# Performance work log

Hardware: AMD Instinct MI355X
Metric: run time of the kernel (lower is better)

Reference implementation:

```python
import jax, jax.numpy as jnp
import numpy as np

B, T, C, H = 4, 2048, 768, 12
D = C // H  # head dim = 64


def setup_inputs() -> dict:
    key = jax.random.key(0)
    ks = jax.random.split(key, 4)
    scale = 0.02
    return {
        "x": jax.random.normal(ks[0], (B, T, C), dtype=jnp.float32),
        "W_attn": jax.random.normal(ks[1], (C, 3 * C), dtype=jnp.float32) * scale,
        "b_attn": jnp.zeros((3 * C,), dtype=jnp.float32),
        "W_proj": jax.random.normal(ks[2], (C, C), dtype=jnp.float32) * scale,
        "b_proj": jnp.zeros((C,), dtype=jnp.float32),
    }


def reference(x, W_attn, b_attn, W_proj, b_proj):
    Bsz, Tlen, Cdim = x.shape
    qkv = x @ W_attn + b_attn                    # [B,T,3C]
    q, k, v = jnp.split(qkv, 3, axis=-1)          # each [B,T,C]
    # [B,T,C] -> [B,H,T,D]
    def heads(t):
        return t.reshape(Bsz, Tlen, H, D).transpose(0, 2, 1, 3)
    q, k, v = heads(q), heads(k), heads(v)
    att = jnp.einsum("bhqd,bhkd->bhqk", q, k) * (1.0 / np.sqrt(D))
    # causal mask: position q attends to k <= q
    mask = jnp.tril(jnp.ones((Tlen, Tlen), dtype=bool))
    att = jnp.where(mask[None, None], att, -jnp.inf)
    att = jax.nn.softmax(att, axis=-1)
    y = jnp.einsum("bhqk,bhkd->bhqd", att, v)     # [B,H,T,D]
    y = y.transpose(0, 2, 1, 3).reshape(Bsz, Tlen, Cdim)
    return y @ W_proj + b_proj
```

## Files before the change

### kernel.cpp

```cpp
#include <hip/hip_runtime.h>

#define B_SZ   4
#define T_LEN  2048
#define C_DIM  768
#define H_NUM  12
#define THREEC (3 * C_DIM)

typedef _Float16 f16;
typedef _Float16 half8 __attribute__((ext_vector_type(8)));
typedef _Float16 half4 __attribute__((ext_vector_type(4)));
typedef __fp16   pk2   __attribute__((ext_vector_type(2)));
typedef float    f32x4 __attribute__((ext_vector_type(4)));

#define GLD16(gaddr, laddr)                                                         \
  __builtin_amdgcn_global_load_lds(                                                 \
      (const __attribute__((address_space(1))) unsigned int*)(gaddr),               \
      (__attribute__((address_space(3))) unsigned int*)(laddr), 16, 0, 0)
#define MFMA16(a, b, c) __builtin_amdgcn_mfma_f32_16x16x32_f16(a, b, c, 0, 0, 0)

__global__ __launch_bounds__(256) void cast_f32_f16_kernel(
    const float* __restrict__ src, f16* __restrict__ dst, int n8) {
  int i = blockIdx.x * 256 + threadIdx.x;
  if (i >= n8) return;
  const float* s = src + (size_t)i * 8;
  half8 h;
#pragma unroll
  for (int u = 0; u < 8; ++u) h[u] = (f16)s[u];
  *(half8*)(dst + (size_t)i * 8) = h;
}

__global__ __launch_bounds__(256) void transpose_cast2_kernel(
    const float* __restrict__ Wa, const float* __restrict__ Wp,
    f16* __restrict__ WtA, f16* __restrict__ WtP) {
  __shared__ f16 tile[32][33];
  int bx = blockIdx.x;
  const float* W; f16* Wt; int N;
  if (bx < THREEC / 32) { W = Wa; Wt = WtA; N = THREEC; }
  else { W = Wp; Wt = WtP; N = C_DIM; bx -= THREEC / 32; }
  const int n0 = bx * 32, k0 = blockIdx.y * 32;
  const int tx = threadIdx.x & 31, ty = threadIdx.x >> 5;
#pragma unroll
  for (int i = 0; i < 4; ++i)
    tile[ty + i * 8][tx] = (f16)W[(size_t)(k0 + ty + i * 8) * N + n0 + tx];
  __syncthreads();
#pragma unroll
  for (int i = 0; i < 4; ++i)
    Wt[(size_t)(n0 + ty + i * 8) * C_DIM + k0 + tx] = tile[tx][ty + i * 8];
}

template <int BM, int BN, int OUT_F16>
__global__ __launch_bounds__(256) void gemm_f16_kernel(
    const f16* __restrict__ A, const f16* __restrict__ Bt,
    const float* __restrict__ bias, f16* __restrict__ OutH,
    float* __restrict__ OutF, int M, int N, int K) {
  __shared__ f16 As[BM * 64];
  __shared__ f16 Bs[BN * 64];
  const int tid = threadIdx.x;
  const int lane = tid & 63, wave = tid >> 6;
  const int lm = lane & 15, kq = lane >> 4, lm7 = lm & 7;
  constexpr int MT = BM / 32, NT = BN / 32;
  const int wm = (wave & 1) * (BM / 2), wn = (wave >> 1) * (BN / 2);
  const int row0 = blockIdx.y * BM, col0 = blockIdx.x * BN;

  f32x4 acc[MT][NT] = {};

  for (int k0 = 0; k0 < K; k0 += 64) {
    __syncthreads();
#pragma unroll
    for (int i = 0; i < BM / 32; ++i) {
      int c = tid + i * 256;
      int r = c >> 3, cc = (c & 7) ^ (r & 7);
      GLD16(&A[(size_t)(row0 + r) * K + k0 + cc * 8],
            &As[(i * 256 + wave * 64) * 8]);
    }
#pragma unroll
    for (int i = 0; i < BN / 32; ++i) {
      int c = tid + i * 256;
      int r = c >> 3, cc = (c & 7) ^ (r & 7);
      GLD16(&Bt[(size_t)(col0 + r) * K + k0 + cc * 8],
            &Bs[(i * 256 + wave * 64) * 8]);
    }
    __syncthreads();
#pragma unroll
    for (int ks = 0; ks < 2; ++ks) {
      const int pos = (ks * 4 + kq);
      half8 af[MT], bf[NT];
#pragma unroll
      for (int t = 0; t < MT; ++t)
        af[t] = *(const half8*)&As[(wm + t * 16 + lm) * 64 + (pos ^ lm7) * 8];
#pragma unroll
      for (int t = 0; t < NT; ++t)
        bf[t] = *(const half8*)&Bs[(wn + t * 16 + lm) * 64 + (pos ^ lm7) * 8];
#pragma unroll
      for (int mt = 0; mt < MT; ++mt)
#pragma unroll
        for (int nt = 0; nt < NT; ++nt)
          acc[mt][nt] = MFMA16(af[mt], bf[nt], acc[mt][nt]);
    }
  }

#pragma unroll
  for (int mt = 0; mt < MT; ++mt) {
    const int row = row0 + wm + mt * 16 + kq * 4;
#pragma unroll
    for (int nt = 0; nt < NT; ++nt) {
      const int col = col0 + wn + nt * 16 + lm;
      const float bv = bias[col];
#pragma unroll
      for (int r = 0; r < 4; ++r) {
        float v = acc[mt][nt][r] + bv;
        if (OUT_F16)
          OutH[(size_t)(row + r) * N + col] = (f16)v;
        else
          OutF[(size_t)(row + r) * N + col] = v;
      }
    }
  }
}

__global__ __launch_bounds__(256) void v_transpose_kernel(
    const f16* __restrict__ qkv, f16* __restrict__ vt) {
  __shared__ f16 tile[64 * 68];
  const int bh = blockIdx.x, b = bh / H_NUM, h = bh % H_NUM;
  const int t0 = blockIdx.y * 64;
  const int tid = threadIdx.x;
#pragma unroll
  for (int i = 0; i < 2; ++i) {
    int c = tid + i * 256;
    int tr = c >> 3, doff = (c & 7) * 8;
    int pcol = ((tr >> 5) << 5) | (((tr >> 2) & 3) << 3) |
               (((tr >> 4) & 1) << 2) | (tr & 3);
    half8 v = *(const half8*)&qkv[(size_t)(b * T_LEN + t0 + tr) * THREEC + 2 * C_DIM + h * 64 + doff];
#pragma unroll
    for (int u = 0; u < 8; ++u) tile[(doff + u) * 68 + pcol] = v[u];
  }
  __syncthreads();
#pragma unroll
  for (int i = 0; i < 2; ++i) {
    int c = tid + i * 256;
    int d = c >> 3, toff = (c & 7) * 8;
    half8 v;
#pragma unroll
    for (int u = 0; u < 8; ++u) v[u] = tile[d * 68 + toff + u];
    *(half8*)&vt[((size_t)bh * 64 + d) * T_LEN + t0 + toff] = v;
  }
}

__global__ __launch_bounds__(512, 8) void attn_kernel(
    const f16* __restrict__ qkv, const f16* __restrict__ vt,
    f16* __restrict__ y) {
  __shared__ f16 Kt[2][64 * 64];
  __shared__ f16 Vt[2][64 * 64];

  const int bh = blockIdx.x, b = bh / H_NUM, h = bh % H_NUM;
  const int yb = blockIdx.y;
  const int qb = 15 - yb;
  const int tid = threadIdx.x, lane = tid & 63, wave = tid >> 6;
  const int lm = lane & 15, kq = lane >> 4, lm7 = lm & 7;
  const int cw = qb * 2 + (wave >> 2);
  const int qw = cw * 64 + (wave & 3) * 16;
  const f16 qscale = (f16)(0.125f * 1.44269504f);

  half8 vones;
#pragma unroll
  for (int u = 0; u < 8; ++u) vones[u] = (f16)1.f;

  half8 bq[2];
#pragma unroll
  for (int c2 = 0; c2 < 2; ++c2) {
    half8 v = *(const half8*)&qkv[(size_t)(b * T_LEN + qw + lm) * THREEC +
                                  h * 64 + c2 * 32 + kq * 8];
    bq[c2] = v * qscale;
  }

  f32x4 o[4] = {};
  f32x4 ol = {};

  f32x4 fz = {};
  asm volatile("" : "+v"(fz));

  const int srow = tid >> 3;
  const int scol = ((tid & 7) ^ (srow & 7)) * 8;
  const f16* kp = &qkv[(size_t)(b * T_LEN + srow) * THREEC + C_DIM + h * 64 + scol];
  const f16* vp = &vt[((size_t)bh * 64 + srow) * T_LEN + scol];

  const int sbase = wave * 512;

  const int n_tiles = qb * 2 + 2;

  GLD16(kp, &Kt[0][sbase]);
  kp += (size_t)64 * THREEC;
  GLD16(vp, &Vt[0][sbase]);
  vp += 64;

  for (int it = 0; it < n_tiles; ++it) {
    const int cur = it & 1;
    if (it + 1 < n_tiles) {
      GLD16(kp, &Kt[cur ^ 1][sbase]);
      kp += (size_t)64 * THREEC;
      GLD16(vp, &Vt[cur ^ 1][sbase]);
      vp += 64;
      asm volatile("s_waitcnt vmcnt(2)" ::: "memory");
    } else {
      asm volatile("s_waitcnt vmcnt(0)" ::: "memory");
    }
    __builtin_amdgcn_s_barrier();

    if (it <= cw) {
      f32x4 s4[4];
#pragma unroll
      for (int ct = 0; ct < 4; ++ct) {
        const f16* kr = &Kt[cur][(ct * 16 + lm) * 64];
        half8 ak0 = *(const half8*)&kr[(kq ^ lm7) * 8];
        half8 ak1 = *(const half8*)&kr[((4 + kq) ^ lm7) * 8];
        f32x4 z = MFMA16(ak0, bq[0], fz);
        s4[ct] = MFMA16(ak1, bq[1], z);
      }
      if (it == cw) {
        const int qrow = qw + lm, j0 = it * 64;
#pragma unroll
        for (int ct = 0; ct < 4; ++ct)
#pragma unroll
          for (int r = 0; r < 4; ++r)
            if (j0 + ct * 16 + kq * 4 + r > qrow) s4[ct][r] = -1e30f;
      }
      union { half8 h8; pk2 p2[4]; } pa0, pa1;
      pa0.p2[0] = __builtin_amdgcn_cvt_pkrtz(
          __builtin_amdgcn_exp2f(s4[0][0]), __builtin_amdgcn_exp2f(s4[0][1]));
      pa0.p2[1] = __builtin_amdgcn_cvt_pkrtz(
          __builtin_amdgcn_exp2f(s4[0][2]), __builtin_amdgcn_exp2f(s4[0][3]));
      pa0.p2[2] = __builtin_amdgcn_cvt_pkrtz(
          __builtin_amdgcn_exp2f(s4[1][0]), __builtin_amdgcn_exp2f(s4[1][1]));
      pa0.p2[3] = __builtin_amdgcn_cvt_pkrtz(
          __builtin_amdgcn_exp2f(s4[1][2]), __builtin_amdgcn_exp2f(s4[1][3]));
      pa1.p2[0] = __builtin_amdgcn_cvt_pkrtz(
          __builtin_amdgcn_exp2f(s4[2][0]), __builtin_amdgcn_exp2f(s4[2][1]));
      pa1.p2[1] = __builtin_amdgcn_cvt_pkrtz(
          __builtin_amdgcn_exp2f(s4[2][2]), __builtin_amdgcn_exp2f(s4[2][3]));
      pa1.p2[2] = __builtin_amdgcn_cvt_pkrtz(
          __builtin_amdgcn_exp2f(s4[3][0]), __builtin_amdgcn_exp2f(s4[3][1]));
      pa1.p2[3] = __builtin_amdgcn_cvt_pkrtz(
          __builtin_amdgcn_exp2f(s4[3][2]), __builtin_amdgcn_exp2f(s4[3][3]));

#pragma unroll
      for (int dt = 0; dt < 4; ++dt) {
        const f16* vr = &Vt[cur][(dt * 16 + lm) * 64];
        half8 bv0 = *(const half8*)&vr[(kq ^ lm7) * 8];
        half8 bv1 = *(const half8*)&vr[((4 + kq) ^ lm7) * 8];
        o[dt] = MFMA16(pa0.h8, bv0, o[dt]);
        o[dt] = MFMA16(pa1.h8, bv1, o[dt]);
      }
      ol = MFMA16(pa0.h8, vones, ol);
      ol = MFMA16(pa1.h8, vones, ol);
    }

    __builtin_amdgcn_s_barrier();
  }

#pragma unroll
  for (int r = 0; r < 4; ++r) {
    const float inv = 1.f / ol[r];
    const size_t base =
        (size_t)(b * T_LEN + qw + kq * 4 + r) * C_DIM + h * 64;
#pragma unroll
    for (int dt = 0; dt < 4; ++dt)
      y[base + dt * 16 + lm] = (f16)(o[dt][r] * inv);
  }
}

extern "C" void kernel_launch(void* const* d_in, const int* in_sizes, int n_in,
                              void* d_out, int out_size, void* d_ws, size_t ws_size,
                              hipStream_t stream) {
  const float* x      = (const float*)d_in[0];
  const float* W_attn = (const float*)d_in[1];
  const float* b_attn = (const float*)d_in[2];
  const float* W_proj = (const float*)d_in[3];
  const float* b_proj = (const float*)d_in[4];
  float* out = (float*)d_out;

  const int M = B_SZ * T_LEN;
  auto align256 = [](size_t v) { return (v + 255) & ~(size_t)255; };
  char* ws = (char*)d_ws;
  f16* xh   = (f16*)ws; ws += align256((size_t)M * C_DIM * 2);
  f16* WtA  = (f16*)ws; ws += align256((size_t)THREEC * C_DIM * 2);
  f16* WtP  = (f16*)ws; ws += align256((size_t)C_DIM * C_DIM * 2);
  f16* qkvh = (f16*)ws; ws += align256((size_t)M * THREEC * 2);
  f16* vtg  = (f16*)ws; ws += align256((size_t)B_SZ * H_NUM * 64 * T_LEN * 2);
  f16* yh   = (f16*)ws; ws += align256((size_t)M * C_DIM * 2);

  {
    int n8 = M * C_DIM / 8;
    cast_f32_f16_kernel<<<(n8 + 255) / 256, 256, 0, stream>>>(x, xh, n8);
  }
  transpose_cast2_kernel<<<dim3((THREEC + C_DIM) / 32, C_DIM / 32), 256, 0, stream>>>(
      W_attn, W_proj, WtA, WtP);

  gemm_f16_kernel<128, 128, 1><<<dim3(THREEC / 128, M / 128), 256, 0, stream>>>(
      xh, WtA, b_attn, qkvh, nullptr, M, THREEC, C_DIM);

  v_transpose_kernel<<<dim3(B_SZ * H_NUM, T_LEN / 64), 256, 0, stream>>>(qkvh, vtg);

  attn_kernel<<<dim3(B_SZ * H_NUM, 16), 512, 0, stream>>>(qkvh, vtg, yh);

  gemm_f16_kernel<128, 64, 0><<<dim3(C_DIM / 64, M / 128), 256, 0, stream>>>(
      yh, WtP, b_proj, nullptr, out, M, C_DIM, C_DIM);
}
```

Baseline: 194.4 us.

## Fuse V transpose into QKV GEMM epilogue and merge prep kernels

The QKV GEMM epilogue now writes the V columns directly into the transposed, permuted per-head layout the attention kernel expects, so the separate v_transpose kernel and its read-back of V are gone. The x cast and the weight transpose-cast are also merged into one prep kernel, which saves a launch. In exchange the V-tile epilogue does scattered half4 stores with stride T_LEN, and V is no longer written to qkvh.

```diff
diff --git a/kernel.cpp b/kernel.cpp
--- a/kernel.cpp
+++ b/kernel.cpp
@@ -5,6 +5,11 @@
 #define C_DIM  768
 #define H_NUM  12
 #define THREEC (3 * C_DIM)
+#define M_ROWS (B_SZ * T_LEN)
+#define CAST_N8 (M_ROWS * C_DIM / 8)
+#define CAST_BLOCKS (CAST_N8 / 256)
+#define TP_BX ((THREEC + C_DIM) / 32)
+#define TP_BY (C_DIM / 32)
 
 typedef _Float16 f16;
 typedef _Float16 half8 __attribute__((ext_vector_type(8)));
@@ -18,26 +23,28 @@
       (__attribute__((address_space(3))) unsigned int*)(laddr), 16, 0, 0)
 #define MFMA16(a, b, c) __builtin_amdgcn_mfma_f32_16x16x32_f16(a, b, c, 0, 0, 0)
 
-__global__ __launch_bounds__(256) void cast_f32_f16_kernel(
-    const float* __restrict__ src, f16* __restrict__ dst, int n8) {
-  int i = blockIdx.x * 256 + threadIdx.x;
-  if (i >= n8) return;
-  const float* s = src + (size_t)i * 8;
-  half8 h;
-#pragma unroll
-  for (int u = 0; u < 8; ++u) h[u] = (f16)s[u];
-  *(half8*)(dst + (size_t)i * 8) = h;
-}
-
-__global__ __launch_bounds__(256) void transpose_cast2_kernel(
+__global__ __launch_bounds__(256) void prep_kernel(
+    const float* __restrict__ x, f16* __restrict__ xh,
     const float* __restrict__ Wa, const float* __restrict__ Wp,
     f16* __restrict__ WtA, f16* __restrict__ WtP) {
   __shared__ f16 tile[32][33];
-  int bx = blockIdx.x;
+  const int bid = blockIdx.x;
+  if (bid < CAST_BLOCKS) {
+    int i = bid * 256 + threadIdx.x;
+    const float* s = x + (size_t)i * 8;
+    half8 h;
+#pragma unroll
+    for (int u = 0; u < 8; ++u) h[u] = (f16)s[u];
+    *(half8*)(xh + (size_t)i * 8) = h;
+    return;
+  }
+  const int t = bid - CAST_BLOCKS;
+  int bx = t % TP_BX;
+  const int by = t / TP_BX;
   const float* W; f16* Wt; int N;
   if (bx < THREEC / 32) { W = Wa; Wt = WtA; N = THREEC; }
   else { W = Wp; Wt = WtP; N = C_DIM; bx -= THREEC / 32; }
-  const int n0 = bx * 32, k0 = blockIdx.y * 32;
+  const int n0 = bx * 32, k0 = by * 32;
   const int tx = threadIdx.x & 31, ty = threadIdx.x >> 5;
 #pragma unroll
   for (int i = 0; i < 4; ++i)
@@ -48,11 +55,11 @@
     Wt[(size_t)(n0 + ty + i * 8) * C_DIM + k0 + tx] = tile[tx][ty + i * 8];
 }
 
-template <int BM, int BN, int OUT_F16>
+template <int BM, int BN, int OUT_F16, int HAS_V>
 __global__ __launch_bounds__(256) void gemm_f16_kernel(
     const f16* __restrict__ A, const f16* __restrict__ Bt,
     const float* __restrict__ bias, f16* __restrict__ OutH,
-    float* __restrict__ OutF, int M, int N, int K) {
+    float* __restrict__ OutF, f16* __restrict__ OutV, int M, int N, int K) {
   __shared__ f16 As[BM * 64];
   __shared__ f16 Bs[BN * 64];
   const int tid = threadIdx.x;
@@ -99,6 +106,30 @@
     }
   }
 
+  if (HAS_V && col0 >= 2 * C_DIM) {
+#pragma unroll
+    for (int mt = 0; mt < MT; ++mt) {
+      const int tt = wm + mt * 16 + kq * 4;
+      const int trow = row0 + tt;
+      const int bb = trow >> 11, tin = trow & (T_LEN - 1);
+      const int m6 = (((tt >> 5) & 1) << 5) | (((tt >> 2) & 3) << 3) |
+                     (((tt >> 4) & 1) << 2);
+      const int tbase = (tin & ~63) | m6;
+#pragma unroll
+      for (int nt = 0; nt < NT; ++nt) {
+        const int col = col0 + wn + nt * 16 + lm;
+        const int dd = col - 2 * C_DIM;
+        const int bh = bb * H_NUM + (dd >> 6);
+        const float bv = bias[col];
+        half4 hv;
+#pragma unroll
+        for (int r = 0; r < 4; ++r) hv[r] = (f16)(acc[mt][nt][r] + bv);
+        *(half4*)&OutV[((size_t)bh * 64 + (dd & 63)) * T_LEN + tbase] = hv;
+      }
+    }
+    return;
+  }
+
 #pragma unroll
   for (int mt = 0; mt < MT; ++mt) {
     const int row = row0 + wm + mt * 16 + kq * 4;
@@ -115,34 +146,6 @@
           OutF[(size_t)(row + r) * N + col] = v;
       }
     }
-  }
-}
-
-__global__ __launch_bounds__(256) void v_transpose_kernel(
-    const f16* __restrict__ qkv, f16* __restrict__ vt) {
-  __shared__ f16 tile[64 * 68];
-  const int bh = blockIdx.x, b = bh / H_NUM, h = bh % H_NUM;
-  const int t0 = blockIdx.y * 64;
-  const int tid = threadIdx.x;
-#pragma unroll
-  for (int i = 0; i < 2; ++i) {
-    int c = tid + i * 256;
-    int tr = c >> 3, doff = (c & 7) * 8;
-    int pcol = ((tr >> 5) << 5) | (((tr >> 2) & 3) << 3) |
-               (((tr >> 4) & 1) << 2) | (tr & 3);
-    half8 v = *(const half8*)&qkv[(size_t)(b * T_LEN + t0 + tr) * THREEC + 2 * C_DIM + h * 64 + doff];
-#pragma unroll
-    for (int u = 0; u < 8; ++u) tile[(doff + u) * 68 + pcol] = v[u];
-  }
-  __syncthreads();
-#pragma unroll
-  for (int i = 0; i < 2; ++i) {
-    int c = tid + i * 256;
-    int d = c >> 3, toff = (c & 7) * 8;
-    half8 v;
-#pragma unroll
-    for (int u = 0; u < 8; ++u) v[u] = tile[d * 68 + toff + u];
-    *(half8*)&vt[((size_t)bh * 64 + d) * T_LEN + t0 + toff] = v;
   }
 }
 
@@ -278,7 +281,7 @@
   const float* b_proj = (const float*)d_in[4];
   float* out = (float*)d_out;
 
-  const int M = B_SZ * T_LEN;
+  const int M = M_ROWS;
   auto align256 = [](size_t v) { return (v + 255) & ~(size_t)255; };
   char* ws = (char*)d_ws;
   f16* xh   = (f16*)ws; ws += align256((size_t)M * C_DIM * 2);
@@ -288,20 +291,14 @@
   f16* vtg  = (f16*)ws; ws += align256((size_t)B_SZ * H_NUM * 64 * T_LEN * 2);
   f16* yh   = (f16*)ws; ws += align256((size_t)M * C_DIM * 2);
 
-  {
-    int n8 = M * C_DIM / 8;
-    cast_f32_f16_kernel<<<(n8 + 255) / 256, 256, 0, stream>>>(x, xh, n8);
-  }
-  transpose_cast2_kernel<<<dim3((THREEC + C_DIM) / 32, C_DIM / 32), 256, 0, stream>>>(
-      W_attn, W_proj, WtA, WtP);
-
-  gemm_f16_kernel<128, 128, 1><<<dim3(THREEC / 128, M / 128), 256, 0, stream>>>(
-      xh, WtA, b_attn, qkvh, nullptr, M, THREEC, C_DIM);
-
-  v_transpose_kernel<<<dim3(B_SZ * H_NUM, T_LEN / 64), 256, 0, stream>>>(qkvh, vtg);
+  prep_kernel<<<CAST_BLOCKS + TP_BX * TP_BY, 256, 0, stream>>>(
+      x, xh, W_attn, W_proj, WtA, WtP);
+
+  gemm_f16_kernel<128, 128, 1, 1><<<dim3(THREEC / 128, M / 128), 256, 0, stream>>>(
+      xh, WtA, b_attn, qkvh, nullptr, vtg, M, THREEC, C_DIM);
 
   attn_kernel<<<dim3(B_SZ * H_NUM, 16), 512, 0, stream>>>(qkvh, vtg, yh);
 
-  gemm_f16_kernel<128, 64, 0><<<dim3(C_DIM / 64, M / 128), 256, 0, stream>>>(
-      yh, WtP, b_proj, nullptr, out, M, C_DIM, C_DIM);
+  gemm_f16_kernel<128, 64, 0, 0><<<dim3(C_DIM / 64, M / 128), 256, 0, stream>>>(
+      yh, WtP, b_proj, nullptr, out, nullptr, M, C_DIM, C_DIM);
 }
```

Result: no change. 195.3 us (+0.5%).
